# Optimization experiments

Measured on AMD Instinct MI355X. Metric: run time of the kernel, lower is better.

## Reference

```python
import jax, jax.numpy as jnp
import numpy as np

D = 1024
N_HEADS = 16
HEAD = D // N_HEADS


def apply_rope(x):
    # x: [b, h, s, hd]
    b, h, s, hd = x.shape
    half = hd // 2
    pos = jnp.arange(1, s + 1, dtype=jnp.float32)  # positions start at 1 (as in source)
    thetas = 10000.0 ** (-2.0 * jnp.arange(half, dtype=jnp.float32) / hd)
    angles = pos[:, None] * thetas[None, :]  # [s, half]
    cos, sin = jnp.cos(angles), jnp.sin(angles)
    x_even, x_odd = x[..., 0::2], x[..., 1::2]
    out_even = x_even * cos - x_odd * sin
    out_odd = x_odd * cos + x_even * sin
    # interleave back: stack on new last axis then reshape
    return jnp.stack([out_even, out_odd], axis=-1).reshape(b, h, s, hd)


def setup_inputs() -> dict:
    key = jax.random.key(0)
    k1, k2, k3 = jax.random.split(key, 3)
    b, s = 4, 2048
    x = jax.random.normal(k1, (b, s, D), dtype=jnp.float32)
    # torch Linear(d, 3d, bias=False): y = x @ W.T; store as [d, 3d] so y = x @ W_qkv
    W_qkv = jax.random.normal(k2, (D, 3 * D), dtype=jnp.float32) * (1.0 / np.sqrt(D))
    W_out = jax.random.normal(k3, (D, D), dtype=jnp.float32) * (1.0 / np.sqrt(D))
    return {"x": x, "W_qkv": W_qkv, "W_out": W_out}


def reference(x, W_qkv, W_out):
    b, s, _ = x.shape
    qkv = x @ W_qkv  # [b, s, 3d]
    q, k, v = jnp.split(qkv, 3, axis=-1)

    def split_heads(t):
        return t.reshape(b, s, N_HEADS, HEAD).transpose(0, 2, 1, 3)  # [b,h,s,hd]

    q, k, v = split_heads(q), split_heads(k), split_heads(v)
    q, k = apply_rope(q), apply_rope(k)
    scale = 1.0 / np.sqrt(HEAD)
    scores = jnp.einsum("bhqd,bhkd->bhqk", q, k) * scale
    attn = jax.nn.softmax(scores, axis=-1)
    out = jnp.einsum("bhqk,bhkd->bhqd", attn, v)  # [b,h,s,hd]
    out = out.transpose(0, 2, 1, 3).reshape(b, s, D)
    return out @ W_out
```

## Files before the change

### kernel.cpp

```cpp
#include <hip/hip_runtime.h>
#include <hip/hip_bf16.h>
#include <math.h>

#define BB 4
#define SS 2048
#define DD 1024
#define NH 16
#define HD 64

typedef __attribute__((ext_vector_type(8))) short bf16x8;
typedef __attribute__((ext_vector_type(4))) float f32x4;

#define MFMA16(a, b, c) __builtin_amdgcn_mfma_f32_16x16x32_bf16(a, b, c, 0, 0, 0)

#if __has_builtin(__builtin_amdgcn_exp2f)
#define EXP2(x) __builtin_amdgcn_exp2f(x)
#else
#define EXP2(x) exp2f(x)
#endif

__device__ __forceinline__ ushort f2bf(float f) {
    unsigned int u = __builtin_bit_cast(unsigned int, f);
    u += 0x7FFF + ((u >> 16) & 1);
    return (ushort)(u >> 16);
}
__device__ __forceinline__ float bf2f(ushort u) {
    return __builtin_bit_cast(float, (unsigned)u << 16);
}
__device__ __forceinline__ unsigned pk2bf(float a, float b) {
    __hip_bfloat162 h = __float22bfloat162_rn(make_float2(a, b));
    unsigned r;
    __builtin_memcpy(&r, &h, 4);
    return r;
}

__device__ __forceinline__ void gload16(const void* g, void* l) {
    __builtin_amdgcn_global_load_lds(
        (const __attribute__((address_space(1))) void*)g,
        (__attribute__((address_space(3))) void*)l, 16, 0, 0);
}

__global__ __launch_bounds__(256)
void cast_x_kernel(const float* __restrict__ X, ushort* __restrict__ Xb)
{
    const size_t i = ((size_t)blockIdx.x * 256 + threadIdx.x) * 8;
    const float4 v0 = *(const float4*)&X[i];
    const float4 v1 = *(const float4*)&X[i + 4];
    uint4 o;
    o.x = (unsigned)f2bf(v0.x) | ((unsigned)f2bf(v0.y) << 16);
    o.y = (unsigned)f2bf(v0.z) | ((unsigned)f2bf(v0.w) << 16);
    o.z = (unsigned)f2bf(v1.x) | ((unsigned)f2bf(v1.y) << 16);
    o.w = (unsigned)f2bf(v1.z) | ((unsigned)f2bf(v1.w) << 16);
    *(uint4*)&Xb[i] = o;
}

template<int NCOLS>
__global__ __launch_bounds__(256)
void castT_kernel(const float* __restrict__ W, ushort* __restrict__ Wt)
{
    __shared__ ushort T[64][72];
    const int blk = blockIdx.x;
    const int ki = blk / (NCOLS / 64), ni = blk % (NCOLS / 64);
    const int k0 = ki * 64, n0 = ni * 64;
    const int t = threadIdx.x;
    #pragma unroll
    for (int e = 0; e < 4; ++e) {
        const int idx = t + e * 256;
        const int kr = idx >> 4, c4 = (idx & 15) * 4;
        const float4 v = *(const float4*)&W[(size_t)(k0 + kr) * NCOLS + n0 + c4];
        T[c4 + 0][kr] = f2bf(v.x); T[c4 + 1][kr] = f2bf(v.y);
        T[c4 + 2][kr] = f2bf(v.z); T[c4 + 3][kr] = f2bf(v.w);
    }
    __syncthreads();
    #pragma unroll
    for (int e = 0; e < 2; ++e) {
        const int idx = t + e * 256;
        const int nr = idx >> 3, kc = (idx & 7) * 8;
        uint4 o;
        o.x = (unsigned)T[nr][kc + 0] | ((unsigned)T[nr][kc + 1] << 16);
        o.y = (unsigned)T[nr][kc + 2] | ((unsigned)T[nr][kc + 3] << 16);
        o.z = (unsigned)T[nr][kc + 4] | ((unsigned)T[nr][kc + 5] << 16);
        o.w = (unsigned)T[nr][kc + 6] | ((unsigned)T[nr][kc + 7] << 16);
        *(uint4*)&Wt[(size_t)(n0 + nr) * 1024 + k0 + kc] = o;
    }
}

__global__ __launch_bounds__(256)
void ropetab_kernel(float2* __restrict__ tab)
{
    const int id = blockIdx.x * 256 + threadIdx.x;
    const int s = id >> 5, i = id & 31;
    const float theta = expf(-0.28782313662425572f * (float)i);
    const float ang = (float)(s + 1) * theta;
    float sn, cs;
    sincosf(ang, &sn, &cs);
    tab[id] = make_float2(cs, sn);
}

__global__ __launch_bounds__(256)
void rope_cast_kernel(ushort* __restrict__ Qi, ushort* __restrict__ Ki,
                      const float2* __restrict__ tab)
{
    const int HALFT = BB * NH * SS * 8;
    const int tid = blockIdx.x * 256 + threadIdx.x;
    const bool isK = tid >= HALFT;
    const int rr = isK ? tid - HALFT : tid;
    ushort* buf = isK ? Ki : Qi;
    const float sc = isK ? 1.0f : 0.180336880111112f;

    const int row = rr >> 3;
    const int e8  = rr & 7;
    const int s   = row & (SS - 1);
    const size_t base = (size_t)row * HD + e8 * 8;
    const uint4 iv = *(const uint4*)&buf[base];
    const unsigned ua[4] = {iv.x, iv.y, iv.z, iv.w};

    uint4 o;
    unsigned ow[4];
    #pragma unroll
    for (int j = 0; j < 4; ++j) {
        const float xe = __builtin_bit_cast(float, ua[j] << 16);
        const float xo = __builtin_bit_cast(float, ua[j] & 0xffff0000u);
        const float2 cs = tab[s * 32 + e8 * 4 + j];
        const float oe = (xe * cs.x - xo * cs.y) * sc;
        const float oo = (xo * cs.x + xe * cs.y) * sc;
        ow[j] = pk2bf(oe, oo);
    }
    o.x = ow[0]; o.y = ow[1]; o.z = ow[2]; o.w = ow[3];
    *(uint4*)&buf[base] = o;
}

template<int K, int NI, int EPI>
__global__ __launch_bounds__(256)
void gemm_bt_kernel(const ushort* __restrict__ Ag, const ushort* __restrict__ Btg,
                    ushort* __restrict__ D0, ushort* __restrict__ D1,
                    ushort* __restrict__ D2, float* __restrict__ Df)
{
    __shared__ ushort Ab[2][128 * 32];
    __shared__ ushort Bb[2][128 * 32];
    const int t = threadIdx.x, lane = t & 63, w = t >> 6;
    const int lo = lane & 15, g = lane >> 4;
    const int wr = w >> 1, wc = w & 1;

    const int nwg = gridDim.x;
    const int bid = blockIdx.x;
    const int wg = (bid & 7) * (nwg >> 3) + (bid >> 3);
    const int m0 = (wg / NI) * 128, n0 = (wg % NI) * 128;

    const int srow  = lane >> 2;
    const int sslot = (lane & 3) ^ ((srow >> 1) & 3);

    f32x4 acc[4][4];
    #pragma unroll
    for (int m = 0; m < 4; ++m)
        #pragma unroll
        for (int n = 0; n < 4; ++n)
            acc[m][n] = (f32x4){0.f, 0.f, 0.f, 0.f};

#define STAGE(kt, bb)                                                              \
    {                                                                              \
        const int kk = (kt) * 32;                                                  \
        _Pragma("unroll")                                                          \
        for (int e = 0; e < 2; ++e) {                                              \
            const int r0 = w * 32 + e * 16;                                        \
            gload16(Ag  + (size_t)(m0 + r0 + srow) * K + kk + sslot * 8,           \
                    &Ab[bb][r0 * 32]);                                             \
            gload16(Btg + (size_t)(n0 + r0 + srow) * K + kk + sslot * 8,           \
                    &Bb[bb][r0 * 32]);                                             \
        }                                                                          \
    }

    const int NKS = K / 32;
    STAGE(0, 0)
    for (int kt = 0; kt < NKS; ++kt) {
        const int cur = kt & 1;
        if (kt + 1 < NKS) {
            STAGE(kt + 1, cur ^ 1)
            asm volatile("s_waitcnt vmcnt(4)" ::: "memory");
        } else {
            asm volatile("s_waitcnt vmcnt(0)" ::: "memory");
        }
        __builtin_amdgcn_sched_barrier(0);
        __builtin_amdgcn_s_barrier();

        const int xsl = ((g ^ ((lo >> 1) & 3)) << 3);
        bf16x8 af[4], bfr[4];
        #pragma unroll
        for (int m = 0; m < 4; ++m)
            af[m] = *(const bf16x8*)&Ab[cur][(wr * 64 + m * 16 + lo) * 32 + xsl];
        #pragma unroll
        for (int n = 0; n < 4; ++n)
            bfr[n] = *(const bf16x8*)&Bb[cur][(wc * 64 + n * 16 + lo) * 32 + xsl];
        #pragma unroll
        for (int m = 0; m < 4; ++m)
            #pragma unroll
            for (int n = 0; n < 4; ++n)
                acc[m][n] = MFMA16(af[m], bfr[n], acc[m][n]);

        asm volatile("s_waitcnt lgkmcnt(0)" ::: "memory");
        __builtin_amdgcn_sched_barrier(0);
        __builtin_amdgcn_s_barrier();
    }
#undef STAGE

    if constexpr (EPI == 0) {
        const int tensor = n0 >> 10;
        const int cb = n0 & 1023;
        if (tensor == 2) {
            #pragma unroll
            for (int m = 0; m < 4; ++m) {
                const int row0 = m0 + wr * 64 + m * 16 + g * 4;
                const int b = row0 >> 11, sbase = row0 & (SS - 1);
                #pragma unroll
                for (int n = 0; n < 4; ++n) {
                    const int c = cb + wc * 64 + n * 16 + lo;
                    const int h = c >> 6, d = c & 63;
                    uint2 wv = make_uint2(pk2bf(acc[m][n][0], acc[m][n][1]),
                                          pk2bf(acc[m][n][2], acc[m][n][3]));
                    *(uint2*)&D2[(((size_t)b * NH + h) * HD + d) * SS + sbase] = wv;
                }
            }
        } else {
            ushort* dst = (tensor == 0) ? D0 : D1;
            const bool evlane = (lo & 1) == 0;
            #pragma unroll
            for (int m = 0; m < 4; ++m)
                #pragma unroll
                for (int n = 0; n < 4; ++n) {
                    const int c = cb + wc * 64 + n * 16 + lo;
                    const int h = c >> 6, d = c & 63;
                    #pragma unroll
                    for (int r = 0; r < 4; ++r) {
                        const int row = m0 + wr * 64 + m * 16 + g * 4 + r;
                        const float x  = acc[m][n][r];
                        const float xp = __shfl_xor(x, 1);
                        if (evlane) {
                            const int b = row >> 11, s = row & (SS - 1);
                            *(unsigned*)&dst[(((size_t)b * NH + h) * SS + s) * HD + d] =
                                pk2bf(x, xp);
                        }
                    }
                }
        }
    } else {
        const bool evlane = (lo & 1) == 0;
        #pragma unroll
        for (int m = 0; m < 4; ++m)
            #pragma unroll
            for (int n = 0; n < 4; ++n) {
                const int col = n0 + wc * 64 + n * 16 + lo;
                #pragma unroll
                for (int r = 0; r < 4; ++r) {
                    const int row = m0 + wr * 64 + m * 16 + g * 4 + r;
                    const float x  = acc[m][n][r];
                    const float xp = __shfl_xor(x, 1);
                    if (evlane)
                        *(float2*)&Df[(size_t)row * 1024 + col] = make_float2(x, xp);
                }
            }
    }
}

__global__ __launch_bounds__(256, 4)
void attn_mfma_kernel(const ushort* __restrict__ Qbf, const ushort* __restrict__ Kbf,
                      const ushort* __restrict__ Vt, ushort* __restrict__ Obt)
{
    __shared__ ushort Ks[2][4096];
    __shared__ ushort Vs[2][4096];
    __shared__ ushort Ps[4][1024];

    const int t    = threadIdx.x;
    const int lane = t & 63;
    const int w    = t >> 6;
    const int g    = lane >> 4;
    const int lo   = lane & 15;
    const int lo7  = lo & 7;
    const int wmask = lo & 6;

    const int i  = blockIdx.x;
    const int r_ = i & 63;
    const int bh = (r_ & 7) * 8 + (r_ >> 3);
    const int qt = i >> 6;

    const size_t kbase  = (size_t)bh * SS * HD;
    const size_t vtbase = (size_t)bh * HD * SS;
    const int s0 = qt * 128;

    bf16x8 qa[2][2];
    #pragma unroll
    for (int qh = 0; qh < 2; ++qh)
        #pragma unroll
        for (int df = 0; df < 2; ++df)
            qa[qh][df] = *(const bf16x8*)
                &Qbf[kbase + (size_t)(s0 + w * 32 + qh * 16 + lo) * HD + df * 32 + g * 8];

    f32x4 Oc[2][4];
    #pragma unroll
    for (int qh = 0; qh < 2; ++qh)
        #pragma unroll
        for (int nb = 0; nb < 4; ++nb)
            Oc[qh][nb] = (f32x4){0.f, 0.f, 0.f, 0.f};
    f32x4 lacc[2];
    lacc[0] = (f32x4){0.f, 0.f, 0.f, 0.f};
    lacc[1] = (f32x4){0.f, 0.f, 0.f, 0.f};
    const bf16x8 ones = {16256, 16256, 16256, 16256, 16256, 16256, 16256, 16256};

    const int srcsw = ((lane & 7) ^ (lane >> 3)) * 8;
    const int rowin = (lane >> 3);

    #define STAGE(kt, bb)                                                          \
    {                                                                              \
        _Pragma("unroll")                                                          \
        for (int e = 0; e < 2; ++e) {                                              \
            const int rw = w * 16 + e * 8;                                         \
            gload16(&Kbf[kbase + (size_t)((kt) * 64 + rw + rowin) * HD + srcsw],   \
                    &Ks[bb][rw * 64]);                                             \
            gload16(&Vt[vtbase + (size_t)(rw + rowin) * SS + (kt) * 64 + srcsw],   \
                    &Vs[bb][rw * 64]);                                             \
        }                                                                          \
    }

    const int NT = SS / 64;
    STAGE(0, 0)

    for (int kt = 0; kt < NT; ++kt) {
        const int cur = kt & 1;
        if (kt + 1 < NT) {
            STAGE(kt + 1, cur ^ 1)
            asm volatile("s_waitcnt vmcnt(4)" ::: "memory");
        } else {
            asm volatile("s_waitcnt vmcnt(0)" ::: "memory");
        }
        __builtin_amdgcn_sched_barrier(0);
        __builtin_amdgcn_s_barrier();

        f32x4 St[2][4];
        __builtin_amdgcn_s_setprio(1);
        #pragma unroll
        for (int k16 = 0; k16 < 4; ++k16) {
            const int row = k16 * 16 + lo;
            const int cb = row * 64;
            const bf16x8 k0 = *(const bf16x8*)&Ks[cur][cb + (((0 + g) ^ lo7) * 8)];
            const bf16x8 k1 = *(const bf16x8*)&Ks[cur][cb + (((4 + g) ^ lo7) * 8)];
            const f32x4 z = {0.f, 0.f, 0.f, 0.f};
            St[0][k16] = MFMA16(k0, qa[0][0], z);
            St[0][k16] = MFMA16(k1, qa[0][1], St[0][k16]);
            St[1][k16] = MFMA16(k0, qa[1][0], z);
            St[1][k16] = MFMA16(k1, qa[1][1], St[1][k16]);
        }
        __builtin_amdgcn_s_setprio(0);

        #pragma unroll
        for (int qh = 0; qh < 2; ++qh)
            #pragma unroll
            for (int k16 = 0; k16 < 4; ++k16)
                #pragma unroll
                for (int r = 0; r < 4; ++r)
                    St[qh][k16][r] = EXP2(St[qh][k16][r]);

        #pragma unroll
        for (int h = 0; h < 2; ++h) {
            #pragma unroll
            for (int qh = 0; qh < 2; ++qh) {
                const int q32 = qh * 16 + lo;
                #pragma unroll
                for (int kr = 0; kr < 2; ++kr) {
                    const f32x4 s4 = St[qh][2 * h + kr];
                    const uint2 wv = make_uint2(pk2bf(s4[0], s4[1]),
                                                pk2bf(s4[2], s4[3]));
                    const int sw = (kr * 4 + g) ^ wmask;
                    *(uint2*)&Ps[w][q32 * 32 + sw * 4] = wv;
                }
            }
            bf16x8 vf[4];
            #pragma unroll
            for (int nb = 0; nb < 4; ++nb)
                vf[nb] = *(const bf16x8*)
                    &Vs[cur][(nb * 16 + lo) * 64 + (((h * 4 + g) ^ lo7) * 8)];
            __builtin_amdgcn_s_setprio(1);
            #pragma unroll
            for (int qh = 0; qh < 2; ++qh) {
                const bf16x8 pa = *(const bf16x8*)
                    &Ps[w][(qh * 16 + lo) * 32 + (((2 * g) ^ wmask) * 4)];
                lacc[qh] = MFMA16(pa, ones, lacc[qh]);
                #pragma unroll
                for (int nb = 0; nb < 4; ++nb)
                    Oc[qh][nb] = MFMA16(pa, vf[nb], Oc[qh][nb]);
            }
            __builtin_amdgcn_s_setprio(0);
        }

        asm volatile("s_waitcnt lgkmcnt(0)" ::: "memory");
        __builtin_amdgcn_sched_barrier(0);
        __builtin_amdgcn_s_barrier();
    }

    const int b = bh >> 4, h = bh & 15;
    #pragma unroll
    for (int qh = 0; qh < 2; ++qh) {
        #pragma unroll
        for (int r = 0; r < 4; ++r) {
            const float inv = 1.0f / lacc[qh][r];
            const int srow = s0 + w * 32 + qh * 16 + g * 4 + r;
            const size_t rbase = (size_t)(b * SS + srow) * 1024 + h * HD;
            #pragma unroll
            for (int nb = 0; nb < 4; ++nb)
                Obt[rbase + nb * 16 + lo] = f2bf(Oc[qh][nb][r] * inv);
        }
    }
    #undef STAGE
}

extern "C" void kernel_launch(void* const* d_in, const int* in_sizes, int n_in,
                              void* d_out, int out_size, void* d_ws, size_t ws_size,
                              hipStream_t stream)
{
    const float* x    = (const float*)d_in[0];
    const float* Wqkv = (const float*)d_in[1];
    const float* Wout = (const float*)d_in[2];
    float* out = (float*)d_out;

    const size_t TEN = (size_t)BB * NH * SS * HD;
    ushort* u = (ushort*)d_ws;
    ushort* Qb16 = u;
    ushort* Kb16 = u + TEN;
    ushort* Vt   = u + 2 * TEN;
    ushort* Obt  = u + 3 * TEN;
    ushort* Xb   = u + 4 * TEN;
    ushort* Wqt  = u + 5 * TEN;
    ushort* Wot  = u + 5 * TEN + 3145728;
    float2* tab  = (float2*)(u + 5 * TEN + 3145728 + 1048576);

    cast_x_kernel<<<dim3(TEN / 2048), 256, 0, stream>>>(x, Xb);
    castT_kernel<3072><<<dim3(16 * 48), 256, 0, stream>>>(Wqkv, Wqt);
    castT_kernel<1024><<<dim3(16 * 16), 256, 0, stream>>>(Wout, Wot);
    ropetab_kernel<<<dim3(SS * 32 / 256), 256, 0, stream>>>(tab);

    gemm_bt_kernel<1024, 24, 0><<<dim3(64 * 24), 256, 0, stream>>>(
        Xb, Wqt, Qb16, Kb16, Vt, nullptr);

    rope_cast_kernel<<<dim3(2 * BB * NH * SS * 8 / 256), 256, 0, stream>>>(
        Qb16, Kb16, tab);

    attn_mfma_kernel<<<dim3(BB * NH * (SS / 128)), 256, 0, stream>>>(
        Qb16, Kb16, Vt, Obt);

    gemm_bt_kernel<1024, 8, 1><<<dim3(64 * 8), 256, 0, stream>>>(
        Obt, Wot, nullptr, nullptr, nullptr, out);
}
```

Before: 212.4 us.

## Give attention warps 64 query rows and add a 128x64-tile output projection GEMM

New measurement: 219.6 us. 1.03x slower.

```diff
diff --git a/kernel.cpp b/kernel.cpp
--- a/kernel.cpp
+++ b/kernel.cpp
@@ -130,11 +130,11 @@
     *(uint4*)&buf[base] = o;
 }
 
-template<int K, int NI, int EPI>
+template<int K, int NI>
 __global__ __launch_bounds__(256)
 void gemm_bt_kernel(const ushort* __restrict__ Ag, const ushort* __restrict__ Btg,
                     ushort* __restrict__ D0, ushort* __restrict__ D1,
-                    ushort* __restrict__ D2, float* __restrict__ Df)
+                    ushort* __restrict__ D2)
 {
     __shared__ ushort Ab[2][128 * 32];
     __shared__ ushort Bb[2][128 * 32];
@@ -203,71 +203,142 @@
     }
 #undef STAGE
 
-    if constexpr (EPI == 0) {
-        const int tensor = n0 >> 10;
-        const int cb = n0 & 1023;
-        if (tensor == 2) {
-            #pragma unroll
-            for (int m = 0; m < 4; ++m) {
-                const int row0 = m0 + wr * 64 + m * 16 + g * 4;
-                const int b = row0 >> 11, sbase = row0 & (SS - 1);
-                #pragma unroll
-                for (int n = 0; n < 4; ++n) {
-                    const int c = cb + wc * 64 + n * 16 + lo;
-                    const int h = c >> 6, d = c & 63;
-                    uint2 wv = make_uint2(pk2bf(acc[m][n][0], acc[m][n][1]),
-                                          pk2bf(acc[m][n][2], acc[m][n][3]));
-                    *(uint2*)&D2[(((size_t)b * NH + h) * HD + d) * SS + sbase] = wv;
-                }
+    const int tensor = n0 >> 10;
+    const int cb = n0 & 1023;
+    if (tensor == 2) {
+        #pragma unroll
+        for (int m = 0; m < 4; ++m) {
+            const int row0 = m0 + wr * 64 + m * 16 + g * 4;
+            const int b = row0 >> 11, sbase = row0 & (SS - 1);
+            #pragma unroll
+            for (int n = 0; n < 4; ++n) {
+                const int c = cb + wc * 64 + n * 16 + lo;
+                const int h = c >> 6, d = c & 63;
+                uint2 wv = make_uint2(pk2bf(acc[m][n][0], acc[m][n][1]),
+                                      pk2bf(acc[m][n][2], acc[m][n][3]));
+                *(uint2*)&D2[(((size_t)b * NH + h) * HD + d) * SS + sbase] = wv;
             }
-        } else {
-            ushort* dst = (tensor == 0) ? D0 : D1;
-            const bool evlane = (lo & 1) == 0;
-            #pragma unroll
-            for (int m = 0; m < 4; ++m)
-                #pragma unroll
-                for (int n = 0; n < 4; ++n) {
-                    const int c = cb + wc * 64 + n * 16 + lo;
-                    const int h = c >> 6, d = c & 63;
-                    #pragma unroll
-                    for (int r = 0; r < 4; ++r) {
-                        const int row = m0 + wr * 64 + m * 16 + g * 4 + r;
-                        const float x  = acc[m][n][r];
-                        const float xp = __shfl_xor(x, 1);
-                        if (evlane) {
-                            const int b = row >> 11, s = row & (SS - 1);
-                            *(unsigned*)&dst[(((size_t)b * NH + h) * SS + s) * HD + d] =
-                                pk2bf(x, xp);
-                        }
-                    }
-                }
         }
     } else {
+        ushort* dst = (tensor == 0) ? D0 : D1;
         const bool evlane = (lo & 1) == 0;
         #pragma unroll
         for (int m = 0; m < 4; ++m)
             #pragma unroll
             for (int n = 0; n < 4; ++n) {
-                const int col = n0 + wc * 64 + n * 16 + lo;
+                const int c = cb + wc * 64 + n * 16 + lo;
+                const int h = c >> 6, d = c & 63;
                 #pragma unroll
                 for (int r = 0; r < 4; ++r) {
                     const int row = m0 + wr * 64 + m * 16 + g * 4 + r;
                     const float x  = acc[m][n][r];
                     const float xp = __shfl_xor(x, 1);
-                    if (evlane)
-                        *(float2*)&Df[(size_t)row * 1024 + col] = make_float2(x, xp);
+                    if (evlane) {
+                        const int b = row >> 11, s = row & (SS - 1);
+                        *(unsigned*)&dst[(((size_t)b * NH + h) * SS + s) * HD + d] =
+                            pk2bf(x, xp);
+                    }
                 }
             }
     }
 }
 
-__global__ __launch_bounds__(256, 4)
+template<int K>
+__global__ __launch_bounds__(256)
+void gemm_bt64_kernel(const ushort* __restrict__ Ag, const ushort* __restrict__ Btg,
+                      float* __restrict__ Df)
+{
+    __shared__ ushort Ab[2][128 * 32];
+    __shared__ ushort Bb[2][64 * 32];
+    const int t = threadIdx.x, lane = t & 63, w = t >> 6;
+    const int lo = lane & 15, g = lane >> 4;
+    const int NI = 16;
+
+    const int nwg = gridDim.x;
+    const int bid = blockIdx.x;
+    const int wg = (bid & 7) * (nwg >> 3) + (bid >> 3);
+    const int m0 = (wg / NI) * 128, n0 = (wg % NI) * 64;
+
+    const int srow  = lane >> 2;
+    const int sslot = (lane & 3) ^ ((srow >> 1) & 3);
+
+    f32x4 acc[2][4];
+    #pragma unroll
+    for (int m = 0; m < 2; ++m)
+        #pragma unroll
+        for (int n = 0; n < 4; ++n)
+            acc[m][n] = (f32x4){0.f, 0.f, 0.f, 0.f};
+
+#define STAGE(kt, bb)                                                              \
+    {                                                                              \
+        const int kk = (kt) * 32;                                                  \
+        _Pragma("unroll")                                                          \
+        for (int e = 0; e < 2; ++e) {                                              \
+            const int r0 = w * 32 + e * 16;                                        \
+            gload16(Ag + (size_t)(m0 + r0 + srow) * K + kk + sslot * 8,            \
+                    &Ab[bb][r0 * 32]);                                             \
+        }                                                                          \
+        gload16(Btg + (size_t)(n0 + w * 16 + srow) * K + kk + sslot * 8,           \
+                &Bb[bb][(w * 16) * 32]);                                           \
+    }
+
+    const int NKS = K / 32;
+    STAGE(0, 0)
+    for (int kt = 0; kt < NKS; ++kt) {
+        const int cur = kt & 1;
+        if (kt + 1 < NKS) {
+            STAGE(kt + 1, cur ^ 1)
+            asm volatile("s_waitcnt vmcnt(3)" ::: "memory");
+        } else {
+            asm volatile("s_waitcnt vmcnt(0)" ::: "memory");
+        }
+        __builtin_amdgcn_sched_barrier(0);
+        __builtin_amdgcn_s_barrier();
+
+        const int xsl = ((g ^ ((lo >> 1) & 3)) << 3);
+        bf16x8 af[2], bfr[4];
+        #pragma unroll
+        for (int m = 0; m < 2; ++m)
+            af[m] = *(const bf16x8*)&Ab[cur][(w * 32 + m * 16 + lo) * 32 + xsl];
+        #pragma unroll
+        for (int n = 0; n < 4; ++n)
+            bfr[n] = *(const bf16x8*)&Bb[cur][(n * 16 + lo) * 32 + xsl];
+        #pragma unroll
+        for (int m = 0; m < 2; ++m)
+            #pragma unroll
+            for (int n = 0; n < 4; ++n)
+                acc[m][n] = MFMA16(af[m], bfr[n], acc[m][n]);
+
+        asm volatile("s_waitcnt lgkmcnt(0)" ::: "memory");
+        __builtin_amdgcn_sched_barrier(0);
+        __builtin_amdgcn_s_barrier();
+    }
+#undef STAGE
+
+    const bool evlane = (lo & 1) == 0;
+    #pragma unroll
+    for (int m = 0; m < 2; ++m)
+        #pragma unroll
+        for (int n = 0; n < 4; ++n) {
+            const int col = n0 + n * 16 + lo;
+            #pragma unroll
+            for (int r = 0; r < 4; ++r) {
+                const int row = m0 + w * 32 + m * 16 + g * 4 + r;
+                const float x  = acc[m][n][r];
+                const float xp = __shfl_xor(x, 1);
+                if (evlane)
+                    *(float2*)&Df[(size_t)row * 1024 + col] = make_float2(x, xp);
+            }
+        }
+}
+
+__global__ __launch_bounds__(128, 2)
 void attn_mfma_kernel(const ushort* __restrict__ Qbf, const ushort* __restrict__ Kbf,
                       const ushort* __restrict__ Vt, ushort* __restrict__ Obt)
 {
     __shared__ ushort Ks[2][4096];
     __shared__ ushort Vs[2][4096];
-    __shared__ ushort Ps[4][1024];
+    __shared__ ushort Ps[2][2048];
 
     const int t    = threadIdx.x;
     const int lane = t & 63;
@@ -275,7 +346,7 @@
     const int g    = lane >> 4;
     const int lo   = lane & 15;
     const int lo7  = lo & 7;
-    const int wmask = lo & 6;
+    const int lo3  = lo & 3;
 
     const int i  = blockIdx.x;
     const int r_ = i & 63;
@@ -286,23 +357,24 @@
     const size_t vtbase = (size_t)bh * HD * SS;
     const int s0 = qt * 128;
 
-    bf16x8 qa[2][2];
-    #pragma unroll
-    for (int qh = 0; qh < 2; ++qh)
+    bf16x8 qa[4][2];
+    #pragma unroll
+    for (int qh = 0; qh < 4; ++qh)
         #pragma unroll
         for (int df = 0; df < 2; ++df)
             qa[qh][df] = *(const bf16x8*)
-                &Qbf[kbase + (size_t)(s0 + w * 32 + qh * 16 + lo) * HD + df * 32 + g * 8];
-
-    f32x4 Oc[2][4];
-    #pragma unroll
-    for (int qh = 0; qh < 2; ++qh)
+                &Qbf[kbase + (size_t)(s0 + w * 64 + qh * 16 + lo) * HD + df * 32 + g * 8];
+
+    f32x4 Oc[4][4];
+    #pragma unroll
+    for (int qh = 0; qh < 4; ++qh)
         #pragma unroll
         for (int nb = 0; nb < 4; ++nb)
             Oc[qh][nb] = (f32x4){0.f, 0.f, 0.f, 0.f};
-    f32x4 lacc[2];
-    lacc[0] = (f32x4){0.f, 0.f, 0.f, 0.f};
-    lacc[1] = (f32x4){0.f, 0.f, 0.f, 0.f};
+    f32x4 lacc[4];
+    #pragma unroll
+    for (int qh = 0; qh < 4; ++qh)
+        lacc[qh] = (f32x4){0.f, 0.f, 0.f, 0.f};
     const bf16x8 ones = {16256, 16256, 16256, 16256, 16256, 16256, 16256, 16256};
 
     const int srcsw = ((lane & 7) ^ (lane >> 3)) * 8;
@@ -311,8 +383,8 @@
     #define STAGE(kt, bb)                                                          \
     {                                                                              \
         _Pragma("unroll")                                                          \
-        for (int e = 0; e < 2; ++e) {                                              \
-            const int rw = w * 16 + e * 8;                                         \
+        for (int e = 0; e < 4; ++e) {                                              \
+            const int rw = w * 32 + e * 8;                                         \
             gload16(&Kbf[kbase + (size_t)((kt) * 64 + rw + rowin) * HD + srcsw],   \
                     &Ks[bb][rw * 64]);                                             \
             gload16(&Vt[vtbase + (size_t)(rw + rowin) * SS + (kt) * 64 + srcsw],   \
@@ -327,61 +399,67 @@
         const int cur = kt & 1;
         if (kt + 1 < NT) {
             STAGE(kt + 1, cur ^ 1)
-            asm volatile("s_waitcnt vmcnt(4)" ::: "memory");
+            asm volatile("s_waitcnt vmcnt(8)" ::: "memory");
         } else {
             asm volatile("s_waitcnt vmcnt(0)" ::: "memory");
         }
         __builtin_amdgcn_sched_barrier(0);
         __builtin_amdgcn_s_barrier();
 
-        f32x4 St[2][4];
+        bf16x8 kf0[4], kf1[4];
+        #pragma unroll
+        for (int k16 = 0; k16 < 4; ++k16) {
+            const int cb = (k16 * 16 + lo) * 64;
+            kf0[k16] = *(const bf16x8*)&Ks[cur][cb + (((0 + g) ^ lo7) * 8)];
+            kf1[k16] = *(const bf16x8*)&Ks[cur][cb + (((4 + g) ^ lo7) * 8)];
+        }
+
+        uint4 pk[4][2];
         __builtin_amdgcn_s_setprio(1);
         #pragma unroll
-        for (int k16 = 0; k16 < 4; ++k16) {
-            const int row = k16 * 16 + lo;
-            const int cb = row * 64;
-            const bf16x8 k0 = *(const bf16x8*)&Ks[cur][cb + (((0 + g) ^ lo7) * 8)];
-            const bf16x8 k1 = *(const bf16x8*)&Ks[cur][cb + (((4 + g) ^ lo7) * 8)];
+        for (int qh = 0; qh < 4; ++qh) {
+            f32x4 St[4];
             const f32x4 z = {0.f, 0.f, 0.f, 0.f};
-            St[0][k16] = MFMA16(k0, qa[0][0], z);
-            St[0][k16] = MFMA16(k1, qa[0][1], St[0][k16]);
-            St[1][k16] = MFMA16(k0, qa[1][0], z);
-            St[1][k16] = MFMA16(k1, qa[1][1], St[1][k16]);
-        }
-        __builtin_amdgcn_s_setprio(0);
-
-        #pragma unroll
-        for (int qh = 0; qh < 2; ++qh)
+            #pragma unroll
+            for (int k16 = 0; k16 < 4; ++k16) {
+                St[k16] = MFMA16(kf0[k16], qa[qh][0], z);
+                St[k16] = MFMA16(kf1[k16], qa[qh][1], St[k16]);
+            }
             #pragma unroll
             for (int k16 = 0; k16 < 4; ++k16)
                 #pragma unroll
                 for (int r = 0; r < 4; ++r)
-                    St[qh][k16][r] = EXP2(St[qh][k16][r]);
-
-        #pragma unroll
-        for (int h = 0; h < 2; ++h) {
-            #pragma unroll
-            for (int qh = 0; qh < 2; ++qh) {
-                const int q32 = qh * 16 + lo;
-                #pragma unroll
-                for (int kr = 0; kr < 2; ++kr) {
-                    const f32x4 s4 = St[qh][2 * h + kr];
-                    const uint2 wv = make_uint2(pk2bf(s4[0], s4[1]),
-                                                pk2bf(s4[2], s4[3]));
-                    const int sw = (kr * 4 + g) ^ wmask;
-                    *(uint2*)&Ps[w][q32 * 32 + sw * 4] = wv;
-                }
+                    St[k16][r] = EXP2(St[k16][r]);
+            #pragma unroll
+            for (int ph = 0; ph < 2; ++ph) {
+                pk[qh][ph].x = pk2bf(St[2 * ph][0],     St[2 * ph][1]);
+                pk[qh][ph].y = pk2bf(St[2 * ph][2],     St[2 * ph][3]);
+                pk[qh][ph].z = pk2bf(St[2 * ph + 1][0], St[2 * ph + 1][1]);
+                pk[qh][ph].w = pk2bf(St[2 * ph + 1][2], St[2 * ph + 1][3]);
             }
+        }
+        __builtin_amdgcn_s_setprio(0);
+
+        #pragma unroll
+        for (int ph = 0; ph < 2; ++ph) {
+            #pragma unroll
+            for (int qh = 0; qh < 4; ++qh)
+                *(uint4*)&Ps[w][(qh * 16 + lo) * 32 + ((g ^ lo3) * 8)] = pk[qh][ph];
             bf16x8 vf[4];
             #pragma unroll
             for (int nb = 0; nb < 4; ++nb)
                 vf[nb] = *(const bf16x8*)
-                    &Vs[cur][(nb * 16 + lo) * 64 + (((h * 4 + g) ^ lo7) * 8)];
+                    &Vs[cur][(nb * 16 + lo) * 64 + (((ph * 4 + g) ^ lo7) * 8)];
             __builtin_amdgcn_s_setprio(1);
             #pragma unroll
-            for (int qh = 0; qh < 2; ++qh) {
-                const bf16x8 pa = *(const bf16x8*)
-                    &Ps[w][(qh * 16 + lo) * 32 + (((2 * g) ^ wmask) * 4)];
+            for (int qh = 0; qh < 4; ++qh) {
+                const int sa = (2 * g) & 3, sb = (2 * g + 1) & 3, p = g >> 1;
+                const int rb = (qh * 16 + lo) * 32;
+                const uint2 ua = *(const uint2*)&Ps[w][rb + ((sa ^ lo3) * 8) + p * 4];
+                const uint2 ub = *(const uint2*)&Ps[w][rb + ((sb ^ lo3) * 8) + p * 4];
+                uint4 pw = make_uint4(ua.x, ua.y, ub.x, ub.y);
+                bf16x8 pa;
+                __builtin_memcpy(&pa, &pw, 16);
                 lacc[qh] = MFMA16(pa, ones, lacc[qh]);
                 #pragma unroll
                 for (int nb = 0; nb < 4; ++nb)
@@ -397,11 +475,11 @@
 
     const int b = bh >> 4, h = bh & 15;
     #pragma unroll
-    for (int qh = 0; qh < 2; ++qh) {
+    for (int qh = 0; qh < 4; ++qh) {
         #pragma unroll
         for (int r = 0; r < 4; ++r) {
             const float inv = 1.0f / lacc[qh][r];
-            const int srow = s0 + w * 32 + qh * 16 + g * 4 + r;
+            const int srow = s0 + w * 64 + qh * 16 + g * 4 + r;
             const size_t rbase = (size_t)(b * SS + srow) * 1024 + h * HD;
             #pragma unroll
             for (int nb = 0; nb < 4; ++nb)
@@ -436,15 +514,14 @@
     castT_kernel<1024><<<dim3(16 * 16), 256, 0, stream>>>(Wout, Wot);
     ropetab_kernel<<<dim3(SS * 32 / 256), 256, 0, stream>>>(tab);
 
-    gemm_bt_kernel<1024, 24, 0><<<dim3(64 * 24), 256, 0, stream>>>(
-        Xb, Wqt, Qb16, Kb16, Vt, nullptr);
+    gemm_bt_kernel<1024, 24><<<dim3(64 * 24), 256, 0, stream>>>(
+        Xb, Wqt, Qb16, Kb16, Vt);
 
     rope_cast_kernel<<<dim3(2 * BB * NH * SS * 8 / 256), 256, 0, stream>>>(
         Qb16, Kb16, tab);
 
-    attn_mfma_kernel<<<dim3(BB * NH * (SS / 128)), 256, 0, stream>>>(
+    attn_mfma_kernel<<<dim3(BB * NH * (SS / 128)), 128, 0, stream>>>(
         Qb16, Kb16, Vt, Obt);
 
-    gemm_bt_kernel<1024, 8, 1><<<dim3(64 * 8), 256, 0, stream>>>(
-        Obt, Wot, nullptr, nullptr, nullptr, out);
-}
+    gemm_bt64_kernel<1024><<<dim3(64 * 16), 256, 0, stream>>>(Obt, Wot, out);
+}
```

## Merge prep kernels into one launch and use 128x64 tiles for output GEMM

Applied to the files above, without the earlier changes.

Result: no change. 209.6 us (-1.3%).

```diff
diff --git a/kernel.cpp b/kernel.cpp
--- a/kernel.cpp
+++ b/kernel.cpp
@@ -41,60 +41,61 @@
 }
 
 __global__ __launch_bounds__(256)
-void cast_x_kernel(const float* __restrict__ X, ushort* __restrict__ Xb)
+void prep_kernel(const float* __restrict__ X, ushort* __restrict__ Xb,
+                 const float* __restrict__ Wqkv, ushort* __restrict__ Wqt,
+                 const float* __restrict__ Wout, ushort* __restrict__ Wot,
+                 float2* __restrict__ tab)
 {
-    const size_t i = ((size_t)blockIdx.x * 256 + threadIdx.x) * 8;
-    const float4 v0 = *(const float4*)&X[i];
-    const float4 v1 = *(const float4*)&X[i + 4];
-    uint4 o;
-    o.x = (unsigned)f2bf(v0.x) | ((unsigned)f2bf(v0.y) << 16);
-    o.y = (unsigned)f2bf(v0.z) | ((unsigned)f2bf(v0.w) << 16);
-    o.z = (unsigned)f2bf(v1.x) | ((unsigned)f2bf(v1.y) << 16);
-    o.w = (unsigned)f2bf(v1.z) | ((unsigned)f2bf(v1.w) << 16);
-    *(uint4*)&Xb[i] = o;
-}
-
-template<int NCOLS>
-__global__ __launch_bounds__(256)
-void castT_kernel(const float* __restrict__ W, ushort* __restrict__ Wt)
-{
-    __shared__ ushort T[64][72];
     const int blk = blockIdx.x;
-    const int ki = blk / (NCOLS / 64), ni = blk % (NCOLS / 64);
-    const int k0 = ki * 64, n0 = ni * 64;
     const int t = threadIdx.x;
-    #pragma unroll
-    for (int e = 0; e < 4; ++e) {
-        const int idx = t + e * 256;
-        const int kr = idx >> 4, c4 = (idx & 15) * 4;
-        const float4 v = *(const float4*)&W[(size_t)(k0 + kr) * NCOLS + n0 + c4];
-        T[c4 + 0][kr] = f2bf(v.x); T[c4 + 1][kr] = f2bf(v.y);
-        T[c4 + 2][kr] = f2bf(v.z); T[c4 + 3][kr] = f2bf(v.w);
-    }
-    __syncthreads();
-    #pragma unroll
-    for (int e = 0; e < 2; ++e) {
-        const int idx = t + e * 256;
-        const int nr = idx >> 3, kc = (idx & 7) * 8;
+    if (blk < 4096) {
+        const size_t i = ((size_t)blk * 256 + t) * 8;
+        const float4 v0 = *(const float4*)&X[i];
+        const float4 v1 = *(const float4*)&X[i + 4];
         uint4 o;
-        o.x = (unsigned)T[nr][kc + 0] | ((unsigned)T[nr][kc + 1] << 16);
-        o.y = (unsigned)T[nr][kc + 2] | ((unsigned)T[nr][kc + 3] << 16);
-        o.z = (unsigned)T[nr][kc + 4] | ((unsigned)T[nr][kc + 5] << 16);
-        o.w = (unsigned)T[nr][kc + 6] | ((unsigned)T[nr][kc + 7] << 16);
-        *(uint4*)&Wt[(size_t)(n0 + nr) * 1024 + k0 + kc] = o;
-    }
-}
-
-__global__ __launch_bounds__(256)
-void ropetab_kernel(float2* __restrict__ tab)
-{
-    const int id = blockIdx.x * 256 + threadIdx.x;
-    const int s = id >> 5, i = id & 31;
-    const float theta = expf(-0.28782313662425572f * (float)i);
-    const float ang = (float)(s + 1) * theta;
-    float sn, cs;
-    sincosf(ang, &sn, &cs);
-    tab[id] = make_float2(cs, sn);
+        o.x = pk2bf(v0.x, v0.y);
+        o.y = pk2bf(v0.z, v0.w);
+        o.z = pk2bf(v1.x, v1.y);
+        o.w = pk2bf(v1.z, v1.w);
+        *(uint4*)&Xb[i] = o;
+    } else if (blk < 5120) {
+        __shared__ ushort T[64][72];
+        const bool isQ = blk < 4864;
+        const int b2 = isQ ? blk - 4096 : blk - 4864;
+        const int ncols = isQ ? 3072 : 1024;
+        const float* W = isQ ? Wqkv : Wout;
+        ushort* Wt = isQ ? Wqt : Wot;
+        const int ki = b2 / (ncols / 64), ni = b2 % (ncols / 64);
+        const int k0 = ki * 64, n0 = ni * 64;
+        #pragma unroll
+        for (int e = 0; e < 4; ++e) {
+            const int idx = t + e * 256;
+            const int kr = idx >> 4, c4 = (idx & 15) * 4;
+            const float4 v = *(const float4*)&W[(size_t)(k0 + kr) * ncols + n0 + c4];
+            T[c4 + 0][kr] = f2bf(v.x); T[c4 + 1][kr] = f2bf(v.y);
+            T[c4 + 2][kr] = f2bf(v.z); T[c4 + 3][kr] = f2bf(v.w);
+        }
+        __syncthreads();
+        #pragma unroll
+        for (int e = 0; e < 2; ++e) {
+            const int idx = t + e * 256;
+            const int nr = idx >> 3, kc = (idx & 7) * 8;
+            uint4 o;
+            o.x = (unsigned)T[nr][kc + 0] | ((unsigned)T[nr][kc + 1] << 16);
+            o.y = (unsigned)T[nr][kc + 2] | ((unsigned)T[nr][kc + 3] << 16);
+            o.z = (unsigned)T[nr][kc + 4] | ((unsigned)T[nr][kc + 5] << 16);
+            o.w = (unsigned)T[nr][kc + 6] | ((unsigned)T[nr][kc + 7] << 16);
+            *(uint4*)&Wt[(size_t)(n0 + nr) * 1024 + k0 + kc] = o;
+        }
+    } else {
+        const int id = (blk - 5120) * 256 + t;
+        const int s = id >> 5, i = id & 31;
+        const float theta = expf(-0.28782313662425572f * (float)i);
+        const float ang = (float)(s + 1) * theta;
+        float sn, cs;
+        sincosf(ang, &sn, &cs);
+        tab[id] = make_float2(cs, sn);
+    }
 }
 
 __global__ __launch_bounds__(256)
@@ -130,11 +131,11 @@
     *(uint4*)&buf[base] = o;
 }
 
-template<int K, int NI, int EPI>
+template<int K, int NI>
 __global__ __launch_bounds__(256)
 void gemm_bt_kernel(const ushort* __restrict__ Ag, const ushort* __restrict__ Btg,
                     ushort* __restrict__ D0, ushort* __restrict__ D1,
-                    ushort* __restrict__ D2, float* __restrict__ Df)
+                    ushort* __restrict__ D2)
 {
     __shared__ ushort Ab[2][128 * 32];
     __shared__ ushort Bb[2][128 * 32];
@@ -203,62 +204,133 @@
     }
 #undef STAGE
 
-    if constexpr (EPI == 0) {
-        const int tensor = n0 >> 10;
-        const int cb = n0 & 1023;
-        if (tensor == 2) {
-            #pragma unroll
-            for (int m = 0; m < 4; ++m) {
-                const int row0 = m0 + wr * 64 + m * 16 + g * 4;
-                const int b = row0 >> 11, sbase = row0 & (SS - 1);
-                #pragma unroll
-                for (int n = 0; n < 4; ++n) {
-                    const int c = cb + wc * 64 + n * 16 + lo;
-                    const int h = c >> 6, d = c & 63;
-                    uint2 wv = make_uint2(pk2bf(acc[m][n][0], acc[m][n][1]),
-                                          pk2bf(acc[m][n][2], acc[m][n][3]));
-                    *(uint2*)&D2[(((size_t)b * NH + h) * HD + d) * SS + sbase] = wv;
-                }
+    const int tensor = n0 >> 10;
+    const int cb = n0 & 1023;
+    if (tensor == 2) {
+        #pragma unroll
+        for (int m = 0; m < 4; ++m) {
+            const int row0 = m0 + wr * 64 + m * 16 + g * 4;
+            const int b = row0 >> 11, sbase = row0 & (SS - 1);
+            #pragma unroll
+            for (int n = 0; n < 4; ++n) {
+                const int c = cb + wc * 64 + n * 16 + lo;
+                const int h = c >> 6, d = c & 63;
+                uint2 wv = make_uint2(pk2bf(acc[m][n][0], acc[m][n][1]),
+                                      pk2bf(acc[m][n][2], acc[m][n][3]));
+                *(uint2*)&D2[(((size_t)b * NH + h) * HD + d) * SS + sbase] = wv;
             }
-        } else {
-            ushort* dst = (tensor == 0) ? D0 : D1;
-            const bool evlane = (lo & 1) == 0;
-            #pragma unroll
-            for (int m = 0; m < 4; ++m)
-                #pragma unroll
-                for (int n = 0; n < 4; ++n) {
-                    const int c = cb + wc * 64 + n * 16 + lo;
-                    const int h = c >> 6, d = c & 63;
-                    #pragma unroll
-                    for (int r = 0; r < 4; ++r) {
-                        const int row = m0 + wr * 64 + m * 16 + g * 4 + r;
-                        const float x  = acc[m][n][r];
-                        const float xp = __shfl_xor(x, 1);
-                        if (evlane) {
-                            const int b = row >> 11, s = row & (SS - 1);
-                            *(unsigned*)&dst[(((size_t)b * NH + h) * SS + s) * HD + d] =
-                                pk2bf(x, xp);
-                        }
-                    }
-                }
         }
     } else {
+        ushort* dst = (tensor == 0) ? D0 : D1;
         const bool evlane = (lo & 1) == 0;
         #pragma unroll
         for (int m = 0; m < 4; ++m)
             #pragma unroll
             for (int n = 0; n < 4; ++n) {
-                const int col = n0 + wc * 64 + n * 16 + lo;
+                const int c = cb + wc * 64 + n * 16 + lo;
+                const int h = c >> 6, d = c & 63;
                 #pragma unroll
                 for (int r = 0; r < 4; ++r) {
                     const int row = m0 + wr * 64 + m * 16 + g * 4 + r;
                     const float x  = acc[m][n][r];
                     const float xp = __shfl_xor(x, 1);
-                    if (evlane)
-                        *(float2*)&Df[(size_t)row * 1024 + col] = make_float2(x, xp);
+                    if (evlane) {
+                        const int b = row >> 11, s = row & (SS - 1);
+                        *(unsigned*)&dst[(((size_t)b * NH + h) * SS + s) * HD + d] =
+                            pk2bf(x, xp);
+                    }
                 }
             }
     }
+}
+
+template<int K>
+__global__ __launch_bounds__(256)
+void gemm_bt64_kernel(const ushort* __restrict__ Ag, const ushort* __restrict__ Btg,
+                      float* __restrict__ Df)
+{
+    __shared__ ushort Ab[2][128 * 32];
+    __shared__ ushort Bb[2][64 * 32];
+    const int t = threadIdx.x, lane = t & 63, w = t >> 6;
+    const int lo = lane & 15, g = lane >> 4;
+    const int NI = 16;
+
+    const int nwg = gridDim.x;
+    const int bid = blockIdx.x;
+    const int wg = (bid & 7) * (nwg >> 3) + (bid >> 3);
+    const int m0 = (wg / NI) * 128, n0 = (wg % NI) * 64;
+
+    const int srow  = lane >> 2;
+    const int sslot = (lane & 3) ^ ((srow >> 1) & 3);
+
+    f32x4 acc[2][4];
+    #pragma unroll
+    for (int m = 0; m < 2; ++m)
+        #pragma unroll
+        for (int n = 0; n < 4; ++n)
+            acc[m][n] = (f32x4){0.f, 0.f, 0.f, 0.f};
+
+#define STAGE(kt, bb)                                                              \
+    {                                                                              \
+        const int kk = (kt) * 32;                                                  \
+        _Pragma("unroll")                                                          \
+        for (int e = 0; e < 2; ++e) {                                              \
+            const int r0 = w * 32 + e * 16;                                        \
+            gload16(Ag + (size_t)(m0 + r0 + srow) * K + kk + sslot * 8,            \
+                    &Ab[bb][r0 * 32]);                                             \
+        }                                                                          \
+        gload16(Btg + (size_t)(n0 + w * 16 + srow) * K + kk + sslot * 8,           \
+                &Bb[bb][(w * 16) * 32]);                                           \
+    }
+
+    const int NKS = K / 32;
+    STAGE(0, 0)
+    for (int kt = 0; kt < NKS; ++kt) {
+        const int cur = kt & 1;
+        if (kt + 1 < NKS) {
+            STAGE(kt + 1, cur ^ 1)
+            asm volatile("s_waitcnt vmcnt(3)" ::: "memory");
+        } else {
+            asm volatile("s_waitcnt vmcnt(0)" ::: "memory");
+        }
+        __builtin_amdgcn_sched_barrier(0);
+        __builtin_amdgcn_s_barrier();
+
+        const int xsl = ((g ^ ((lo >> 1) & 3)) << 3);
+        bf16x8 af[2], bfr[4];
+        #pragma unroll
+        for (int m = 0; m < 2; ++m)
+            af[m] = *(const bf16x8*)&Ab[cur][(w * 32 + m * 16 + lo) * 32 + xsl];
+        #pragma unroll
+        for (int n = 0; n < 4; ++n)
+            bfr[n] = *(const bf16x8*)&Bb[cur][(n * 16 + lo) * 32 + xsl];
+        #pragma unroll
+        for (int m = 0; m < 2; ++m)
+            #pragma unroll
+            for (int n = 0; n < 4; ++n)
+                acc[m][n] = MFMA16(af[m], bfr[n], acc[m][n]);
+
+        asm volatile("s_waitcnt lgkmcnt(0)" ::: "memory");
+        __builtin_amdgcn_sched_barrier(0);
+        __builtin_amdgcn_s_barrier();
+    }
+#undef STAGE
+
+    const bool evlane = (lo & 1) == 0;
+    #pragma unroll
+    for (int m = 0; m < 2; ++m)
+        #pragma unroll
+        for (int n = 0; n < 4; ++n) {
+            const int col = n0 + n * 16 + lo;
+            #pragma unroll
+            for (int r = 0; r < 4; ++r) {
+                const int row = m0 + w * 32 + m * 16 + g * 4 + r;
+                const float x  = acc[m][n][r];
+                const float xp = __shfl_xor(x, 1);
+                if (evlane)
+                    *(float2*)&Df[(size_t)row * 1024 + col] = make_float2(x, xp);
+            }
+        }
 }
 
 __global__ __launch_bounds__(256, 4)
@@ -431,13 +503,11 @@
     ushort* Wot  = u + 5 * TEN + 3145728;
     float2* tab  = (float2*)(u + 5 * TEN + 3145728 + 1048576);
 
-    cast_x_kernel<<<dim3(TEN / 2048), 256, 0, stream>>>(x, Xb);
-    castT_kernel<3072><<<dim3(16 * 48), 256, 0, stream>>>(Wqkv, Wqt);
-    castT_kernel<1024><<<dim3(16 * 16), 256, 0, stream>>>(Wout, Wot);
-    ropetab_kernel<<<dim3(SS * 32 / 256), 256, 0, stream>>>(tab);
-
-    gemm_bt_kernel<1024, 24, 0><<<dim3(64 * 24), 256, 0, stream>>>(
-        Xb, Wqt, Qb16, Kb16, Vt, nullptr);
+    prep_kernel<<<dim3(4096 + 768 + 256 + 256), 256, 0, stream>>>(
+        x, Xb, Wqkv, Wqt, Wout, Wot, tab);
+
+    gemm_bt_kernel<1024, 24><<<dim3(64 * 24), 256, 0, stream>>>(
+        Xb, Wqt, Qb16, Kb16, Vt);
 
     rope_cast_kernel<<<dim3(2 * BB * NH * SS * 8 / 256), 256, 0, stream>>>(
         Qb16, Kb16, tab);
@@ -445,6 +515,5 @@
     attn_mfma_kernel<<<dim3(BB * NH * (SS / 128)), 256, 0, stream>>>(
         Qb16, Kb16, Vt, Obt);
 
-    gemm_bt_kernel<1024, 8, 1><<<dim3(64 * 8), 256, 0, stream>>>(
-        Obt, Wot, nullptr, nullptr, nullptr, out);
-}
+    gemm_bt64_kernel<1024><<<dim3(64 * 16), 256, 0, stream>>>(Obt, Wot, out);
+}
```
